# Kernel optimization log

Measured on AMD Instinct MI355X. Metric: run time of the kernel, lower is better.

## Reference

```python
import jax, jax.numpy as jnp
import numpy as np

B, L, H, T_MAX, D_ID, D_SZ, D_POS = 64, 1024, 256, 128, 128, 64, 128
V_ID, V_SZ = 65536, 256


def setup_inputs() -> dict:
    key = jax.random.key(0)
    ks = jax.random.split(key, 16)
    s = 0.02
    inp = {
        'obj_id': jax.random.randint(ks[0], (B,), 0, V_ID, dtype=jnp.int32),
        'obj_size': jax.random.randint(ks[1], (B,), 0, V_SZ, dtype=jnp.int32),
        'cache_lines': jax.random.randint(ks[2], (B, L), 0, V_ID, dtype=jnp.int32),
        'lengths': jax.random.randint(ks[3], (B,), 0, L, dtype=jnp.int32),
        'c0': jax.random.normal(ks[4], (B, H), jnp.float32),
        'h0': jax.random.normal(ks[5], (B, H), jnp.float32),
        'history': jax.random.normal(ks[6], (B, T_MAX - 1, H), jnp.float32),
        # learned parameters
        'obj_id_table': jax.random.normal(ks[7], (V_ID, D_ID), jnp.float32) * s,
        'obj_size_table': jax.random.normal(ks[8], (V_SZ, D_SZ), jnp.float32) * s,
        'pos_table': jax.random.normal(ks[9], (T_MAX, D_POS), jnp.float32) * s,
        'W_ih': jax.random.normal(ks[10], (4 * H, D_ID + D_SZ), jnp.float32) * s,
        'W_hh': jax.random.normal(ks[11], (4 * H, H), jnp.float32) * s,
        'b_ih': jnp.zeros((4 * H,), jnp.float32),
        'b_hh': jnp.zeros((4 * H,), jnp.float32),
        'attn_W': jax.random.normal(ks[12], (D_ID, H), jnp.float32) * s,
        'scorer_W': jax.random.normal(ks[13], (1, H + D_POS), jnp.float32) * s,
        'scorer_b': jnp.zeros((1,), jnp.float32),
        'reuse_W': jax.random.normal(ks[14], (1, H + D_POS), jnp.float32) * s,
        'reuse_b': jnp.zeros((1,), jnp.float32),
    }
    return inp


def reference(obj_id, obj_size, cache_lines, lengths, c0, h0, history,
              obj_id_table, obj_size_table, pos_table,
              W_ih, W_hh, b_ih, b_hh, attn_W,
              scorer_W, scorer_b, reuse_W, reuse_b):
    # --- embed current access and run one LSTMCell step ---
    x = jnp.concatenate([obj_id_table[obj_id], obj_size_table[obj_size]], axis=-1)  # (B, D_ID+D_SZ)
    gates = x @ W_ih.T + b_ih + h0 @ W_hh.T + b_hh  # (B, 4H)
    i, f, g, o = jnp.split(gates, 4, axis=-1)
    c = jax.nn.sigmoid(f) * c0 + jax.nn.sigmoid(i) * jnp.tanh(g)
    h = jax.nn.sigmoid(o) * jnp.tanh(c)

    # --- growing hidden-state history (deque bounded at max_attention_history) ---
    hist = jnp.concatenate([history, h[:, None, :]], axis=1)  # (B, T, H)
    T = hist.shape[1]
    pos = jnp.broadcast_to(pos_table[:T][None], (hist.shape[0], T, pos_table.shape[1]))
    values = jnp.concatenate([hist, pos], axis=-1)  # (B, T, H+P)

    # --- cache line embeddings (cache_lines_embedder == obj_id_embedder) ---
    q = obj_id_table[cache_lines]  # (B, L, D_ID)

    # --- General (bilinear) multi-query attention over history ---
    scores = jnp.einsum('bld,dh,bth->blt', q, attn_W, hist)  # (B, L, T)
    weights = jax.nn.softmax(scores, axis=-1)
    contexts = jnp.einsum('blt,btv->blv', weights, values)  # (B, L, H+P)

    # --- heads ---
    line_scores = jax.nn.softmax((contexts @ scorer_W.T + scorer_b)[..., 0], axis=-1)  # (B, L)
    pred_reuse = (contexts @ reuse_W.T + reuse_b)[..., 0]  # (B, L)

    # --- mask_renormalize over valid (unpadded) cache lines ---
    valid = jnp.maximum(lengths, 1)[:, None]  # min_len=1 in pad()
    mask = (jnp.arange(line_scores.shape[1])[None, :] < valid).astype(line_scores.dtype)
    masked = line_scores * mask
    denom = masked.sum(axis=-1, keepdims=True)
    probs = masked / jnp.where(denom > 0, denom, 1.0)
    return probs, pred_reuse
```

## Files before the change

kernel.cpp:

```cpp
#include <hip/hip_runtime.h>
#include <math.h>

#define BB 64
#define LL 1024
#define HH 256
#define TT 128
#define D_ID 128
#define D_SZ 64
#define D_POS 128
#define DX 192

typedef short s16x8 __attribute__((ext_vector_type(8)));
typedef float f32x16 __attribute__((ext_vector_type(16)));
typedef unsigned short u16x8 __attribute__((ext_vector_type(8)));
typedef unsigned short u16x4 __attribute__((ext_vector_type(4)));

__device__ __forceinline__ unsigned short f2bf(float f) {
    unsigned u = __float_as_uint(f);
    unsigned r = u + 0x7fffu + ((u >> 16) & 1u);
    return (unsigned short)(r >> 16);
}

__device__ __forceinline__ s16x8 pack8(float4 a, float4 b) {
    u16x8 p;
    p[0] = f2bf(a.x); p[1] = f2bf(a.y); p[2] = f2bf(a.z); p[3] = f2bf(a.w);
    p[4] = f2bf(b.x); p[5] = f2bf(b.y); p[6] = f2bf(b.z); p[7] = f2bf(b.w);
    return (s16x8)p;
}

__global__ void embed_kernel(const int* __restrict__ obj_id,
                             const int* __restrict__ obj_size,
                             const float* __restrict__ h0,
                             const float* __restrict__ obj_id_table,
                             const float* __restrict__ obj_size_table,
                             const float* __restrict__ history,
                             const float* __restrict__ attn_W,
                             float* __restrict__ xh_t,
                             unsigned short* __restrict__ qT,
                             unsigned short* __restrict__ histB,
                             unsigned short* __restrict__ attnWB) {
    int blk = blockIdx.x;
    int tid = threadIdx.x;

    if (blk < 112) {
        int b = tid & 63;
        int k = blk * 4 + (tid >> 6);
        float v;
        if (k < D_ID)      v = obj_id_table[(size_t)obj_id[b] * D_ID + k];
        else if (k < DX)   v = obj_size_table[(size_t)obj_size[b] * D_SZ + (k - D_ID)];
        else               v = h0[b * HH + (k - DX)];
        xh_t[k * 64 + b] = v;
        return;
    }
    if (blk < 4208) {
        size_t g = ((size_t)(blk - 112) * 256 + tid) * 8;
        float4 a = *(const float4*)(obj_id_table + g);
        float4 b = *(const float4*)(obj_id_table + g + 4);
        *(s16x8*)(qT + g) = pack8(a, b);
        return;
    }
    if (blk < 5224) {
        size_t g = ((size_t)(blk - 4208) * 256 + tid) * 8;
        float4 a = *(const float4*)(history + g);
        float4 b = *(const float4*)(history + g + 4);
        *(s16x8*)(histB + g) = pack8(a, b);
        return;
    }
    {
        size_t g = ((size_t)(blk - 5224) * 256 + tid) * 8;
        float4 a = *(const float4*)(attn_W + g);
        float4 b = *(const float4*)(attn_W + g + 4);
        *(s16x8*)(attnWB + g) = pack8(a, b);
    }
}

__global__ void gates_kernel(const float* __restrict__ xh_t,
                             const float* __restrict__ W_ih,
                             const float* __restrict__ W_hh,
                             const float* __restrict__ b_ih,
                             const float* __restrict__ b_hh,
                             const float* __restrict__ c0,
                             float* __restrict__ h_new,
                             unsigned short* __restrict__ hnewB) {
    int j = blockIdx.x;
    int tid = threadIdx.x;
    int b = tid & 63;
    int q = __builtin_amdgcn_readfirstlane(tid >> 6);
    int r = q * HH + j;
    __shared__ float gS[256];

    float acc = b_ih[r] + b_hh[r];
    const float* wi = W_ih + (size_t)r * DX;
    const float* wh = W_hh + (size_t)r * HH;
#pragma unroll 16
    for (int k = 0; k < DX; ++k)
        acc += wi[k] * xh_t[k * 64 + b];
#pragma unroll 16
    for (int k = 0; k < HH; ++k)
        acc += wh[k] * xh_t[(DX + k) * 64 + b];
    gS[q * 64 + b] = acc;
    __syncthreads();

    if (tid < 64) {
        float ig = 1.f / (1.f + expf(-gS[tid]));
        float fg = 1.f / (1.f + expf(-gS[64 + tid]));
        float gg = tanhf(gS[128 + tid]);
        float og = 1.f / (1.f + expf(-gS[192 + tid]));
        float c = fg * c0[tid * HH + j] + ig * gg;
        float h = og * tanhf(c);
        h_new[tid * HH + j] = h;
        hnewB[tid * HH + j] = f2bf(h);
    }
}

__global__ void proj_kernel(const unsigned short* __restrict__ histB,
                            const unsigned short* __restrict__ hnewB,
                            const float* __restrict__ history,
                            const float* __restrict__ h_new,
                            const unsigned short* __restrict__ attnWB,
                            const float* __restrict__ pos_table,
                            const float* __restrict__ scorer_W,
                            const float* __restrict__ reuse_W,
                            unsigned short* __restrict__ hpF,
                            float* __restrict__ sv,
                            float* __restrict__ rv) {
    int blk = blockIdx.x;
    int tid = threadIdx.x;

    if (blk >= 256) {
        int b = blk - 256;
        int which = tid >> 7;
        int t = tid & 127;
        const float* w = which ? reuse_W : scorer_W;
        const float* hrow = (t < TT - 1)
            ? history + ((size_t)b * (TT - 1) + t) * HH
            : h_new + (size_t)b * HH;
        float acc = 0.f;
#pragma unroll 8
        for (int k = 0; k < HH / 4; ++k) {
            float4 hv = *(const float4*)(hrow + 4 * k);
            float4 wv = *(const float4*)(w + 4 * k);
            acc += hv.x * wv.x + hv.y * wv.y + hv.z * wv.z + hv.w * wv.w;
        }
        const float* prow = pos_table + (size_t)t * D_POS;
#pragma unroll 8
        for (int k = 0; k < D_POS / 4; ++k) {
            float4 pv = *(const float4*)(prow + 4 * k);
            float4 wv = *(const float4*)(w + HH + 4 * k);
            acc += pv.x * wv.x + pv.y * wv.y + pv.z * wv.z + pv.w * wv.w;
        }
        (which ? rv : sv)[b * TT + t] = acc;
        return;
    }

    int b  = blk >> 2;
    int tt = blk & 3;
    int w  = tid >> 6;
    int lane = tid & 63;
    int ln = lane & 31, half = lane >> 5;

    int t = tt * 32 + ln;
    const unsigned short* arow = attnWB + (size_t)(32 * w + ln) * HH;
    const unsigned short* brow = (t < TT - 1)
        ? histB + ((size_t)b * (TT - 1) + t) * HH
        : hnewB + (size_t)b * HH;

    f32x16 acc;
#pragma unroll
    for (int r = 0; r < 16; ++r) acc[r] = 0.f;

#pragma unroll
    for (int ks = 0; ks < 16; ++ks) {
        int off = ks * 16 + half * 8;
        s16x8 af = *(const s16x8*)(arow + off);
        s16x8 bf = *(const s16x8*)(brow + off);
        acc = __builtin_amdgcn_mfma_f32_32x32x16_bf16(af, bf, acc, 0, 0, 0);
    }

    unsigned short* hb = hpF + (size_t)b * 16384;
#pragma unroll
    for (int qd = 0; qd < 4; ++qd) {
        u16x4 v;
        v[0] = f2bf(acc[4 * qd + 0]);
        v[1] = f2bf(acc[4 * qd + 1]);
        v[2] = f2bf(acc[4 * qd + 2]);
        v[3] = f2bf(acc[4 * qd + 3]);
        int sa = ((2 * w + (qd >> 1)) * 4 + tt) * 512 +
                 (qd & 1) * 256 + ln * 8 + 4 * half;
        *(u16x4*)(hb + sa) = v;
    }
}

__global__ void __launch_bounds__(64)
attn_kernel(const int* __restrict__ cache_lines,
            const unsigned short* __restrict__ qT,
            const unsigned short* __restrict__ hpF,
            const float* __restrict__ sv,
            const float* __restrict__ rv,
            const float* __restrict__ scorer_b,
            const float* __restrict__ reuse_b,
            float* __restrict__ logits,
            float* __restrict__ out_reuse) {
    int b  = blockIdx.x >> 5;
    int l0 = (blockIdx.x & 31) * 32;
    int lane = threadIdx.x;
    int ln = lane & 31, half = lane >> 5;

    int cl = cache_lines[b * LL + l0 + ln];
    const unsigned short* qrow = qT + (size_t)cl * D_ID + half * 8;
    s16x8 qf[8];
#pragma unroll
    for (int ks = 0; ks < 8; ++ks)
        qf[ks] = *(const s16x8*)(qrow + ks * 16);

    float sb = scorer_b[0], rb = reuse_b[0];

    const s16x8* hpb = (const s16x8*)(hpF) + (size_t)b * 2048;
    f32x16 acc[4];
#pragma unroll
    for (int tt = 0; tt < 4; ++tt)
#pragma unroll
        for (int r = 0; r < 16; ++r) acc[tt][r] = 0.f;

#pragma unroll
    for (int k = 0; k < 8; ++k) {
#pragma unroll
        for (int tt = 0; tt < 4; ++tt) {
            s16x8 bf = hpb[(k * 4 + tt) * 64 + lane];
            acc[tt] = __builtin_amdgcn_mfma_f32_32x32x16_bf16(bf, qf[k], acc[tt], 0, 0, 0);
        }
    }

    float m = -1e30f;
#pragma unroll
    for (int tt = 0; tt < 4; ++tt)
#pragma unroll
        for (int r = 0; r < 16; ++r) m = fmaxf(m, acc[tt][r]);
    m = fmaxf(m, __shfl_xor(m, 32));

    float s = 0.f, lg = 0.f, rg = 0.f;
#pragma unroll
    for (int tt = 0; tt < 4; ++tt) {
#pragma unroll
        for (int q = 0; q < 4; ++q) {
            const float4 s4 = *(const float4*)(sv + b * TT + tt * 32 + 8 * q + 4 * half);
            const float4 r4 = *(const float4*)(rv + b * TT + tt * 32 + 8 * q + 4 * half);
            float e0 = __expf(acc[tt][4 * q + 0] - m);
            float e1 = __expf(acc[tt][4 * q + 1] - m);
            float e2 = __expf(acc[tt][4 * q + 2] - m);
            float e3 = __expf(acc[tt][4 * q + 3] - m);
            s  += e0 + e1 + e2 + e3;
            lg += e0 * s4.x + e1 * s4.y + e2 * s4.z + e3 * s4.w;
            rg += e0 * r4.x + e1 * r4.y + e2 * r4.z + e3 * r4.w;
        }
    }
    s  += __shfl_xor(s, 32);
    lg += __shfl_xor(lg, 32);
    rg += __shfl_xor(rg, 32);

    if (half == 0) {
        logits[b * LL + l0 + ln] = lg / s + sb;
        out_reuse[b * LL + l0 + ln] = rg / s + rb;
    }
}

__global__ void finalsm_kernel(const float* __restrict__ logits,
                               const int* __restrict__ lengths,
                               float* __restrict__ out_probs) {
    int b = blockIdx.x;
    int tid = threadIdx.x;
    int valid = max(lengths[b], 1);
    float v[4];
    float m = -1e30f;
#pragma unroll
    for (int i = 0; i < 4; ++i) {
        int l = tid + 256 * i;
        v[i] = (l < valid) ? logits[b * LL + l] : -1e30f;
        m = fmaxf(m, v[i]);
    }
#pragma unroll
    for (int off = 1; off < 64; off <<= 1) m = fmaxf(m, __shfl_xor(m, off));
    __shared__ float redm[4];
    __shared__ float reds[4];
    int wave = tid >> 6;
    if ((tid & 63) == 0) redm[wave] = m;
    __syncthreads();
    m = fmaxf(fmaxf(redm[0], redm[1]), fmaxf(redm[2], redm[3]));
    float e[4];
    float s = 0.f;
#pragma unroll
    for (int i = 0; i < 4; ++i) {
        int l = tid + 256 * i;
        e[i] = (l < valid) ? expf(v[i] - m) : 0.f;
        s += e[i];
    }
#pragma unroll
    for (int off = 1; off < 64; off <<= 1) s += __shfl_xor(s, off);
    if ((tid & 63) == 0) reds[wave] = s;
    __syncthreads();
    s = reds[0] + reds[1] + reds[2] + reds[3];
    float inv = 1.f / s;
#pragma unroll
    for (int i = 0; i < 4; ++i)
        out_probs[b * LL + tid + 256 * i] = e[i] * inv;
}

extern "C" void kernel_launch(void* const* d_in, const int* in_sizes, int n_in,
                              void* d_out, int out_size, void* d_ws, size_t ws_size,
                              hipStream_t stream) {
    const int*   obj_id         = (const int*)d_in[0];
    const int*   obj_size       = (const int*)d_in[1];
    const int*   cache_lines    = (const int*)d_in[2];
    const int*   lengths        = (const int*)d_in[3];
    const float* c0             = (const float*)d_in[4];
    const float* h0             = (const float*)d_in[5];
    const float* history        = (const float*)d_in[6];
    const float* obj_id_table   = (const float*)d_in[7];
    const float* obj_size_table = (const float*)d_in[8];
    const float* pos_table      = (const float*)d_in[9];
    const float* W_ih           = (const float*)d_in[10];
    const float* W_hh           = (const float*)d_in[11];
    const float* b_ih           = (const float*)d_in[12];
    const float* b_hh           = (const float*)d_in[13];
    const float* attn_W         = (const float*)d_in[14];
    const float* scorer_W       = (const float*)d_in[15];
    const float* scorer_b       = (const float*)d_in[16];
    const float* reuse_W        = (const float*)d_in[17];
    const float* reuse_b        = (const float*)d_in[18];

    float* out = (float*)d_out;
    float* out_probs = out;
    float* out_reuse = out + BB * LL;

    char* ws = (char*)d_ws;
    float*          h_new  = (float*)(ws);
    unsigned short* hpF    = (unsigned short*)(ws + 65536);
    float*          sv     = (float*)(ws + 2162688);
    float*          rv     = (float*)(ws + 2195456);
    float*          xh_t   = (float*)(ws + 2228224);
    float*          logits = (float*)(ws + 2228224);
    unsigned short* qT     = (unsigned short*)(ws + 4194304);
    unsigned short* histB  = (unsigned short*)(ws + 20971520);
    unsigned short* attnWB = (unsigned short*)(ws + 25165824);
    unsigned short* hnewB  = (unsigned short*)(ws + 25231360);

    hipLaunchKernelGGL(embed_kernel, dim3(5240), dim3(256), 0, stream,
                       obj_id, obj_size, h0, obj_id_table, obj_size_table,
                       history, attn_W, xh_t, qT, histB, attnWB);
    hipLaunchKernelGGL(gates_kernel, dim3(HH), dim3(256), 0, stream,
                       xh_t, W_ih, W_hh, b_ih, b_hh, c0, h_new, hnewB);
    hipLaunchKernelGGL(proj_kernel, dim3(320), dim3(256), 0, stream,
                       histB, hnewB, history, h_new, attnWB, pos_table,
                       scorer_W, reuse_W, hpF, sv, rv);
    hipLaunchKernelGGL(attn_kernel, dim3(BB * 32), dim3(64), 0, stream,
                       cache_lines, qT, hpF, sv, rv,
                       scorer_b, reuse_b, logits, out_reuse);
    hipLaunchKernelGGL(finalsm_kernel, dim3(BB), dim3(256), 0, stream,
                       logits, lengths, out_probs);
}
```

Measured before the change: 171.8 us.

## Gather and convert only referenced embedding rows instead of the full table to bf16

Removes the bulk fp32-to-bf16 conversion of the full 65536x128 obj_id table, the history tensor and attn_W. Instead, the projection kernel gathers only the rows referenced by cache_lines into a per-tile, MFMA-fragment-ordered bf16 buffer, and converts history and attn_W on the fly inside the MFMA loop. Traffic for the table conversion drops from the whole table (32MB read plus 16MB written) to about 32MB read plus 16MB written for the gathered rows. The projection kernel now reads fp32 operands directly and repeats the conversion work per wave.

```diff
diff --git a/kernel.cpp b/kernel.cpp
--- a/kernel.cpp
+++ b/kernel.cpp
@@ -33,45 +33,15 @@
                              const float* __restrict__ h0,
                              const float* __restrict__ obj_id_table,
                              const float* __restrict__ obj_size_table,
-                             const float* __restrict__ history,
-                             const float* __restrict__ attn_W,
-                             float* __restrict__ xh_t,
-                             unsigned short* __restrict__ qT,
-                             unsigned short* __restrict__ histB,
-                             unsigned short* __restrict__ attnWB) {
-    int blk = blockIdx.x;
+                             float* __restrict__ xh_t) {
     int tid = threadIdx.x;
-
-    if (blk < 112) {
-        int b = tid & 63;
-        int k = blk * 4 + (tid >> 6);
-        float v;
-        if (k < D_ID)      v = obj_id_table[(size_t)obj_id[b] * D_ID + k];
-        else if (k < DX)   v = obj_size_table[(size_t)obj_size[b] * D_SZ + (k - D_ID)];
-        else               v = h0[b * HH + (k - DX)];
-        xh_t[k * 64 + b] = v;
-        return;
-    }
-    if (blk < 4208) {
-        size_t g = ((size_t)(blk - 112) * 256 + tid) * 8;
-        float4 a = *(const float4*)(obj_id_table + g);
-        float4 b = *(const float4*)(obj_id_table + g + 4);
-        *(s16x8*)(qT + g) = pack8(a, b);
-        return;
-    }
-    if (blk < 5224) {
-        size_t g = ((size_t)(blk - 4208) * 256 + tid) * 8;
-        float4 a = *(const float4*)(history + g);
-        float4 b = *(const float4*)(history + g + 4);
-        *(s16x8*)(histB + g) = pack8(a, b);
-        return;
-    }
-    {
-        size_t g = ((size_t)(blk - 5224) * 256 + tid) * 8;
-        float4 a = *(const float4*)(attn_W + g);
-        float4 b = *(const float4*)(attn_W + g + 4);
-        *(s16x8*)(attnWB + g) = pack8(a, b);
-    }
+    int b = tid & 63;
+    int k = blockIdx.x * 4 + (tid >> 6);
+    float v;
+    if (k < D_ID)      v = obj_id_table[(size_t)obj_id[b] * D_ID + k];
+    else if (k < DX)   v = obj_size_table[(size_t)obj_size[b] * D_SZ + (k - D_ID)];
+    else               v = h0[b * HH + (k - DX)];
+    xh_t[k * 64 + b] = v;
 }
 
 __global__ void gates_kernel(const float* __restrict__ xh_t,
@@ -80,8 +50,7 @@
                              const float* __restrict__ b_ih,
                              const float* __restrict__ b_hh,
                              const float* __restrict__ c0,
-                             float* __restrict__ h_new,
-                             unsigned short* __restrict__ hnewB) {
+                             float* __restrict__ h_new) {
     int j = blockIdx.x;
     int tid = threadIdx.x;
     int b = tid & 63;
@@ -107,30 +76,89 @@
         float gg = tanhf(gS[128 + tid]);
         float og = 1.f / (1.f + expf(-gS[192 + tid]));
         float c = fg * c0[tid * HH + j] + ig * gg;
-        float h = og * tanhf(c);
-        h_new[tid * HH + j] = h;
-        hnewB[tid * HH + j] = f2bf(h);
-    }
-}
-
-__global__ void proj_kernel(const unsigned short* __restrict__ histB,
-                            const unsigned short* __restrict__ hnewB,
+        h_new[tid * HH + j] = og * tanhf(c);
+    }
+}
+
+__global__ void proj_kernel(const int* __restrict__ cache_lines,
+                            const float* __restrict__ obj_id_table,
                             const float* __restrict__ history,
                             const float* __restrict__ h_new,
-                            const unsigned short* __restrict__ attnWB,
+                            const float* __restrict__ attn_W,
                             const float* __restrict__ pos_table,
                             const float* __restrict__ scorer_W,
                             const float* __restrict__ reuse_W,
+                            unsigned short* __restrict__ qG,
                             unsigned short* __restrict__ hpF,
                             float* __restrict__ sv,
                             float* __restrict__ rv) {
     int blk = blockIdx.x;
     int tid = threadIdx.x;
 
-    if (blk >= 256) {
-        int b = blk - 256;
-        int which = tid >> 7;
-        int t = tid & 127;
+    if (blk < 2048) {
+        int tile = blk;
+        int b = tile >> 5, l0 = (tile & 31) * 32;
+        int ln = tid & 31, half = tid >> 5;
+        int cl = cache_lines[b * LL + l0 + ln];
+        const float* qrow = obj_id_table + (size_t)cl * D_ID;
+        unsigned short* dst = qG + (size_t)tile * 4096;
+#pragma unroll
+        for (int ks = 0; ks < 8; ++ks) {
+            float4 a = *(const float4*)(qrow + ks * 16 + half * 8);
+            float4 c = *(const float4*)(qrow + ks * 16 + half * 8 + 4);
+            *(s16x8*)(dst + (ks * 64 + tid) * 8) = pack8(a, c);
+        }
+        return;
+    }
+
+    if (blk < 3072) {
+        int p = blk - 2048;
+        int b  = p >> 4;
+        int w  = (p >> 2) & 3;
+        int tt = p & 3;
+        int ln = tid & 31, half = tid >> 5;
+
+        int t = tt * 32 + ln;
+        const float* arow = attn_W + (size_t)(32 * w + ln) * HH;
+        const float* brow = (t < TT - 1)
+            ? history + ((size_t)b * (TT - 1) + t) * HH
+            : h_new + (size_t)b * HH;
+
+        f32x16 acc;
+#pragma unroll
+        for (int r = 0; r < 16; ++r) acc[r] = 0.f;
+
+#pragma unroll
+        for (int ks = 0; ks < 16; ++ks) {
+            int off = ks * 16 + half * 8;
+            float4 a0 = *(const float4*)(arow + off);
+            float4 a1 = *(const float4*)(arow + off + 4);
+            float4 b0 = *(const float4*)(brow + off);
+            float4 b1 = *(const float4*)(brow + off + 4);
+            acc = __builtin_amdgcn_mfma_f32_32x32x16_bf16(
+                pack8(a0, a1), pack8(b0, b1), acc, 0, 0, 0);
+        }
+
+        unsigned short* hb = hpF + (size_t)b * 16384;
+#pragma unroll
+        for (int qd = 0; qd < 4; ++qd) {
+            u16x4 v;
+            v[0] = f2bf(acc[4 * qd + 0]);
+            v[1] = f2bf(acc[4 * qd + 1]);
+            v[2] = f2bf(acc[4 * qd + 2]);
+            v[3] = f2bf(acc[4 * qd + 3]);
+            int sa = ((2 * w + (qd >> 1)) * 4 + tt) * 512 +
+                     (qd & 1) * 256 + ln * 8 + 4 * half;
+            *(u16x4*)(hb + sa) = v;
+        }
+        return;
+    }
+
+    {
+        int idx = blk - 3072;
+        int b = idx >> 2;
+        int which = (idx >> 1) & 1;
+        int t = (idx & 1) * 64 + tid;
         const float* w = which ? reuse_W : scorer_W;
         const float* hrow = (t < TT - 1)
             ? history + ((size_t)b * (TT - 1) + t) * HH
@@ -150,50 +178,11 @@
             acc += pv.x * wv.x + pv.y * wv.y + pv.z * wv.z + pv.w * wv.w;
         }
         (which ? rv : sv)[b * TT + t] = acc;
-        return;
-    }
-
-    int b  = blk >> 2;
-    int tt = blk & 3;
-    int w  = tid >> 6;
-    int lane = tid & 63;
-    int ln = lane & 31, half = lane >> 5;
-
-    int t = tt * 32 + ln;
-    const unsigned short* arow = attnWB + (size_t)(32 * w + ln) * HH;
-    const unsigned short* brow = (t < TT - 1)
-        ? histB + ((size_t)b * (TT - 1) + t) * HH
-        : hnewB + (size_t)b * HH;
-
-    f32x16 acc;
-#pragma unroll
-    for (int r = 0; r < 16; ++r) acc[r] = 0.f;
-
-#pragma unroll
-    for (int ks = 0; ks < 16; ++ks) {
-        int off = ks * 16 + half * 8;
-        s16x8 af = *(const s16x8*)(arow + off);
-        s16x8 bf = *(const s16x8*)(brow + off);
-        acc = __builtin_amdgcn_mfma_f32_32x32x16_bf16(af, bf, acc, 0, 0, 0);
-    }
-
-    unsigned short* hb = hpF + (size_t)b * 16384;
-#pragma unroll
-    for (int qd = 0; qd < 4; ++qd) {
-        u16x4 v;
-        v[0] = f2bf(acc[4 * qd + 0]);
-        v[1] = f2bf(acc[4 * qd + 1]);
-        v[2] = f2bf(acc[4 * qd + 2]);
-        v[3] = f2bf(acc[4 * qd + 3]);
-        int sa = ((2 * w + (qd >> 1)) * 4 + tt) * 512 +
-                 (qd & 1) * 256 + ln * 8 + 4 * half;
-        *(u16x4*)(hb + sa) = v;
     }
 }
 
 __global__ void __launch_bounds__(64)
-attn_kernel(const int* __restrict__ cache_lines,
-            const unsigned short* __restrict__ qT,
+attn_kernel(const unsigned short* __restrict__ qG,
             const unsigned short* __restrict__ hpF,
             const float* __restrict__ sv,
             const float* __restrict__ rv,
@@ -201,17 +190,17 @@
             const float* __restrict__ reuse_b,
             float* __restrict__ logits,
             float* __restrict__ out_reuse) {
-    int b  = blockIdx.x >> 5;
-    int l0 = (blockIdx.x & 31) * 32;
+    int tile = blockIdx.x;
+    int b  = tile >> 5;
+    int l0 = (tile & 31) * 32;
     int lane = threadIdx.x;
     int ln = lane & 31, half = lane >> 5;
 
-    int cl = cache_lines[b * LL + l0 + ln];
-    const unsigned short* qrow = qT + (size_t)cl * D_ID + half * 8;
+    const s16x8* qsrc = (const s16x8*)(qG) + (size_t)tile * 512;
     s16x8 qf[8];
 #pragma unroll
     for (int ks = 0; ks < 8; ++ks)
-        qf[ks] = *(const s16x8*)(qrow + ks * 16);
+        qf[ks] = qsrc[ks * 64 + lane];
 
     float sb = scorer_b[0], rb = reuse_b[0];
 
@@ -339,22 +328,17 @@
     float*          rv     = (float*)(ws + 2195456);
     float*          xh_t   = (float*)(ws + 2228224);
     float*          logits = (float*)(ws + 2228224);
-    unsigned short* qT     = (unsigned short*)(ws + 4194304);
-    unsigned short* histB  = (unsigned short*)(ws + 20971520);
-    unsigned short* attnWB = (unsigned short*)(ws + 25165824);
-    unsigned short* hnewB  = (unsigned short*)(ws + 25231360);
-
-    hipLaunchKernelGGL(embed_kernel, dim3(5240), dim3(256), 0, stream,
-                       obj_id, obj_size, h0, obj_id_table, obj_size_table,
-                       history, attn_W, xh_t, qT, histB, attnWB);
+    unsigned short* qG     = (unsigned short*)(ws + 4194304);
+
+    hipLaunchKernelGGL(embed_kernel, dim3(112), dim3(256), 0, stream,
+                       obj_id, obj_size, h0, obj_id_table, obj_size_table, xh_t);
     hipLaunchKernelGGL(gates_kernel, dim3(HH), dim3(256), 0, stream,
-                       xh_t, W_ih, W_hh, b_ih, b_hh, c0, h_new, hnewB);
-    hipLaunchKernelGGL(proj_kernel, dim3(320), dim3(256), 0, stream,
-                       histB, hnewB, history, h_new, attnWB, pos_table,
-                       scorer_W, reuse_W, hpF, sv, rv);
+                       xh_t, W_ih, W_hh, b_ih, b_hh, c0, h_new);
+    hipLaunchKernelGGL(proj_kernel, dim3(3328), dim3(64), 0, stream,
+                       cache_lines, obj_id_table, history, h_new, attn_W,
+                       pos_table, scorer_W, reuse_W, qG, hpF, sv, rv);
     hipLaunchKernelGGL(attn_kernel, dim3(BB * 32), dim3(64), 0, stream,
-                       cache_lines, qT, hpF, sv, rv,
-                       scorer_b, reuse_b, logits, out_reuse);
+                       qG, hpF, sv, rv, scorer_b, reuse_b, logits, out_reuse);
     hipLaunchKernelGGL(finalsm_kernel, dim3(BB), dim3(256), 0, stream,
                        logits, lengths, out_probs);
 }
```

New measurement: 163.0 us. -5.1%, faster.
